# Kernel tuning notes

Measured on AMD Instinct MI355X. Metric: run time of the kernel, lower is better.

The kernel has to match this reference:

```python
import jax, jax.numpy as jnp
import numpy as np

EPS = 1e-5

def _quant_w(w):
    # symmetric per-tensor 8-bit weight quantization with straight-through estimator
    s = jnp.max(jnp.abs(w)) / 127.0
    wq = jnp.round(jnp.clip(w / s, -127.0, 127.0)) * s
    return w + jax.lax.stop_gradient(wq - w)

def _adder_conv(x, w, stride):
    # AdderNet conv: out[b,co,ow] = -sum_{cin,k} |x[b,cin,ow*stride+k] - w[co,cin,k]|
    # x: (B, Cin, L), w: (Co, Cin, K)
    B, Cin, L = x.shape
    Co, _, K = w.shape
    Ow = (L - K) // stride + 1
    idx = jnp.arange(Ow)[:, None] * stride + jnp.arange(K)[None, :]      # (Ow, K)
    patches = x[:, :, idx]                                               # (B, Cin, Ow, K)
    diff = jnp.abs(patches[:, None] - w[None, :, :, None, :])            # (B, Co, Cin, Ow, K)
    return -diff.sum(axis=(2, 4))                                        # (B, Co, Ow)

def _bn(x, p):
    # eval-mode BatchNorm; x: (B,C,W), p: (4,C) = [gamma, beta, running_mean, running_var]
    g, b, m, v = p
    return (x - m[:, None]) * (g[:, None] * jax.lax.rsqrt(v[:, None] + EPS)) + b[:, None]

def _bn_params(key, c):
    k1, k2, k3, k4 = jax.random.split(key, 4)
    g = jax.random.uniform(k1, (c,)) + 0.5
    b = 0.1 * jax.random.normal(k2, (c,))
    m = 0.1 * jax.random.normal(k3, (c,))
    v = jax.random.uniform(k4, (c,)) + 0.5
    return jnp.stack([g, b, m, v]).astype(jnp.float32)

def setup_inputs() -> dict:
    key = jax.random.key(0)
    ks = jax.random.split(key, 22)
    B = 8192
    w = lambda k, shp: (0.1 * jax.random.normal(k, shp)).astype(jnp.float32)
    return {
        'x': jax.random.normal(ks[0], (B, 1, 1, 256), dtype=jnp.float32),
        'w_pre1': w(ks[1], (5, 1, 13)),   'bn_pre1': _bn_params(ks[2], 5),
        'w_pre2': w(ks[3], (10, 5, 9)),   'bn_pre2': _bn_params(ks[4], 10),
        'w_r1':   w(ks[5], (10, 10, 1)),  'bn_r1':   _bn_params(ks[6], 10),
        'w_r2':   w(ks[7], (10, 10, 1)),  'bn_r2':   _bn_params(ks[8], 10),
        'w_o1a':  w(ks[9], (70, 140, 1)), 'bn_o1a':  _bn_params(ks[10], 70),
        'w_o1b':  w(ks[11], (30, 70, 1)), 'bn_o1b':  _bn_params(ks[12], 30),
        'w_o1c':  w(ks[13], (1, 30, 1)),  'bn_o1c':  _bn_params(ks[14], 1),
        'w_o2a':  w(ks[15], (70, 140, 1)),'bn_o2a':  _bn_params(ks[16], 70),
        'w_o2b':  w(ks[17], (30, 70, 1)), 'bn_o2b':  _bn_params(ks[18], 30),
        'w_o2c':  w(ks[19], (1, 30, 1)),  'bn_o2c':  _bn_params(ks[20], 1),
    }

def reference(x, w_pre1, bn_pre1, w_pre2, bn_pre2, w_r1, bn_r1, w_r2, bn_r2,
              w_o1a, bn_o1a, w_o1b, bn_o1b, w_o1c, bn_o1c,
              w_o2a, bn_o2a, w_o2b, bn_o2b, w_o2c, bn_o2c):
    relu = jax.nn.relu
    B = x.shape[0]
    h = x.reshape(B, 1, 256)                                  # height dim is 1 -> 1D
    h = relu(_bn(_adder_conv(h, _quant_w(w_pre1), 5), bn_pre1))   # (B,5,49)
    h = relu(_bn(_adder_conv(h, _quant_w(w_pre2), 3), bn_pre2))   # (B,10,14)
    # ResBlock
    t = relu(_bn(_adder_conv(h, _quant_w(w_r1), 1), bn_r1))
    t = _bn(_adder_conv(t, _quant_w(w_r2), 1), bn_r2)
    h = relu(t + h)                                           # (B,10,14)
    f = h.reshape(B, 140, 1)                                  # flatten to channels
    # O1 branch (amplitude-weighted average lifetime)
    a = relu(_bn(_adder_conv(f, _quant_w(w_o1a), 1), bn_o1a))
    a = relu(_bn(_adder_conv(a, _quant_w(w_o1b), 1), bn_o1b))
    a = relu(_bn(_adder_conv(a, _quant_w(w_o1c), 1), bn_o1c))
    tau_amp = a.reshape(-1)                                   # (B,)
    # O2 branch (intensity-weighted average lifetime)
    b = relu(_bn(_adder_conv(f, _quant_w(w_o2a), 1), bn_o2a))
    b = relu(_bn(_adder_conv(b, _quant_w(w_o2b), 1), bn_o2b))
    b = relu(_bn(_adder_conv(b, _quant_w(w_o2c), 1), bn_o2c))
    tau_inten = b.reshape(-1)                                 # (B,)
    return (tau_amp, tau_inten)
```

## Files before the change

kernel.cpp:

```cpp
#include <hip/hip_runtime.h>

#define TPB 256
#define EPB 8
#define H1S 246
#define ES  280

#define WQ1   0
#define WQ2   65
#define WR1Q  515
#define WR2Q  615
#define WCQ   715
#define WSB   779
#define SMALL_N 1253
#define WQAT  1280
#define WQBT  20880

#define SB_P1 0
#define SB_P2 10
#define SB_R1 30
#define SB_R2 50
#define SB_A1 70
#define SB_B1 210
#define SB_C1 270
#define SB_A2 272
#define SB_B2 412
#define SB_C2 472

#define GFOLD(bn, C, OFF)                                                     \
  if (tid < (C)) {                                                            \
    float gg = (bn)[tid], bb = (bn)[(C) + tid];                               \
    float mm = (bn)[2 * (C) + tid], vv = (bn)[3 * (C) + tid];                 \
    float sc = gg / sqrtf(vv + 1e-5f);                                        \
    sbp[(OFF) + tid] = sc;                                                    \
    sbp[(OFF) + (C) + tid] = bb - mm * sc;                                    \
  }

extern "C" __global__ __launch_bounds__(256)
void prep(const float* __restrict__ w1,  const float* __restrict__ bnp1,
          const float* __restrict__ w2,  const float* __restrict__ bnp2,
          const float* __restrict__ wr1, const float* __restrict__ bnr1,
          const float* __restrict__ wr2, const float* __restrict__ bnr2,
          const float* __restrict__ wa1, const float* __restrict__ bna1,
          const float* __restrict__ wb1, const float* __restrict__ bnb1,
          const float* __restrict__ wc1, const float* __restrict__ bnc1,
          const float* __restrict__ wa2, const float* __restrict__ bna2,
          const float* __restrict__ wb2, const float* __restrict__ bnb2,
          const float* __restrict__ wc2, const float* __restrict__ bnc2,
          float* __restrict__ ws)
{
  __shared__ float s_red[4];
  const int tid = threadIdx.x;
  const int b = blockIdx.x;

  if (b == 10) {
    float* sbp = ws + WSB;
    GFOLD(bnp1, 5, SB_P1)  GFOLD(bnp2, 10, SB_P2)
    GFOLD(bnr1, 10, SB_R1) GFOLD(bnr2, 10, SB_R2)
    GFOLD(bna1, 70, SB_A1) GFOLD(bnb1, 30, SB_B1) GFOLD(bnc1, 1, SB_C1)
    GFOLD(bna2, 70, SB_A2) GFOLD(bnb2, 30, SB_B2) GFOLD(bnc2, 1, SB_C2)
    return;
  }

  const float* src; int n; int mode; int rofs; float* dst = ws;
  int ofs = 0;
  switch (b) {
    case 0: src = w1;  ofs = WQ1;      n = 65;   mode = 0; rofs = 0;  break;
    case 1: src = w2;  ofs = WQ2;      n = 450;  mode = 0; rofs = 0;  break;
    case 2: src = wr1; ofs = WR1Q;     n = 100;  mode = 0; rofs = 0;  break;
    case 3: src = wr2; ofs = WR2Q;     n = 100;  mode = 0; rofs = 0;  break;
    case 4: src = wa1; ofs = WQAT;     n = 9800; mode = 1; rofs = 0;  break;
    case 5: src = wb1; ofs = WQBT;     n = 2100; mode = 2; rofs = 0;  break;
    case 6: src = wc1; ofs = WCQ;      n = 30;   mode = 0; rofs = 0;  break;
    case 7: src = wa2; ofs = WQAT;     n = 9800; mode = 1; rofs = 70; break;
    case 8: src = wb2; ofs = WQBT;     n = 2100; mode = 2; rofs = 30; break;
    default:src = wc2; ofs = WCQ + 32; n = 30;   mode = 0; rofs = 0;  break;
  }

  float m = 0.f;
  for (int i = tid; i < n; i += 256) m = fmaxf(m, fabsf(src[i]));
#pragma unroll
  for (int off = 32; off > 0; off >>= 1)
    m = fmaxf(m, __shfl_down(m, off, 64));
  if ((tid & 63) == 0) s_red[tid >> 6] = m;
  __syncthreads();
  m = fmaxf(fmaxf(s_red[0], s_red[1]), fmaxf(s_red[2], s_red[3]));

  float s = m / 127.0f;
  for (int i = tid; i < n; i += 256) {
    float w = src[i];
    float q = rintf(fminf(fmaxf(w / s, -127.f), 127.f)) * s;
    if (mode == 0) {
      dst[ofs + i] = q;
    } else if (mode == 1) {
      int r = i / 140 + rofs, c = i % 140;
      dst[ofs + ((c >> 2) * 140 + r) * 4 + (c & 3)] = q;
    } else {
      int r = i / 70 + rofs, c = i % 70;
      dst[ofs + ((c >> 1) * 60 + r) * 2 + (c & 1)] = q;
    }
  }
}

extern "C" __global__ __launch_bounds__(TPB, 4)
void taunet(const float* __restrict__ x, const float* __restrict__ ws,
            float* __restrict__ out, int B)
{
  __shared__ __align__(16) float s_h1[EPB * H1S];
  __shared__ __align__(16) float s_e[EPB * ES];
  __shared__ __align__(16) float s_small[SMALL_N];

  const int tid = threadIdx.x;
  const int g  = tid >> 5;
  const int l  = tid & 31;
  const int ln = tid & 63;
  const int wv = tid >> 6;
  const int gp = 2 * wv;
  const int elem = blockIdx.x * EPB + g;

  for (int i = ln; i < SMALL_N; i += 64) s_small[i] = ws[i];

  {
    const float4* xb = (const float4*)x;
#pragma unroll
    for (int it = 0; it < 2; ++it) {
      int e = gp + it;
      int ge = blockIdx.x * EPB + e;
      if (ge < B) {
        float4 v = xb[ge * 64 + ln];
        *(float4*)&s_e[e * ES + ln * 4] = v;
      }
    }
  }

  const float* sb = &s_small[WSB];

  {
    const float* xe = &s_e[g * ES];
#pragma unroll
    for (int rep = 0; rep < 2; ++rep) {
      int p = l + 32 * rep;
      bool act = p < 49;
      int ps = act ? p : 0;
      float win[13];
#pragma unroll
      for (int k = 0; k < 13; ++k) win[k] = xe[5 * ps + k];
#pragma unroll
      for (int ci = 0; ci < 5; ++ci) {
        float a0 = 0.f, a1 = 0.f;
#pragma unroll
        for (int k = 0; k < 13; ++k) {
          float d = fabsf(win[k] - s_small[WQ1 + ci * 13 + k]);
          if (k & 1) a1 += d; else a0 += d;
        }
        float v = fmaxf(fmaf(-(a0 + a1), sb[SB_P1 + ci], sb[SB_P1 + 5 + ci]), 0.f);
        if (act) s_h1[g * H1S + ci * 49 + ps] = v;
      }
    }
  }

  {
    const int ch = l >> 4;
    const int ow16 = l & 15;
    const bool act = ow16 < 14;
    const int ow = act ? ow16 : 0;
    const float* h1b = &s_h1[g * H1S];
    float acc[5] = {0.f, 0.f, 0.f, 0.f, 0.f};
#pragma unroll
    for (int ci = 0; ci < 5; ++ci) {
      float w9[9];
#pragma unroll
      for (int k = 0; k < 9; ++k) w9[k] = h1b[ci * 49 + 3 * ow + k];
#pragma unroll
      for (int c = 0; c < 5; ++c) {
        int co = ch * 5 + c;
        float s0 = 0.f, s1 = 0.f;
#pragma unroll
        for (int k = 0; k < 9; ++k) {
          float d = fabsf(w9[k] - s_small[WQ2 + co * 45 + ci * 9 + k]);
          if (k & 1) s1 += d; else s0 += d;
        }
        acc[c] += s0 + s1;
      }
    }
#pragma unroll
    for (int c = 0; c < 5; ++c) {
      int co = ch * 5 + c;
      float v = fmaxf(fmaf(-acc[c], sb[SB_P2 + co], sb[SB_P2 + 10 + co]), 0.f);
      if (act) s_e[g * ES + co * 14 + ow] = v;
    }
  }

#pragma unroll
  for (int j = 0; j < 5; ++j) {
    int idx = l + 32 * j;
    if (idx < 140) {
      int co = idx / 14, ow = idx % 14;
      float a0 = 0.f, a1 = 0.f;
#pragma unroll
      for (int ci = 0; ci < 10; ++ci) {
        float d = fabsf(s_e[g * ES + ci * 14 + ow] - s_small[WR1Q + co * 10 + ci]);
        if (ci & 1) a1 += d; else a0 += d;
      }
      s_e[g * ES + 140 + idx] =
          fmaxf(fmaf(-(a0 + a1), sb[SB_R1 + co], sb[SB_R1 + 10 + co]), 0.f);
    }
  }

#pragma unroll
  for (int j = 0; j < 5; ++j) {
    int idx = l + 32 * j;
    if (idx < 140) {
      int co = idx / 14, ow = idx % 14;
      float a0 = 0.f, a1 = 0.f;
#pragma unroll
      for (int ci = 0; ci < 10; ++ci) {
        float d = fabsf(s_e[g * ES + 140 + ci * 14 + ow] - s_small[WR2Q + co * 10 + ci]);
        if (ci & 1) a1 += d; else a0 += d;
      }
      float t2 = fmaf(-(a0 + a1), sb[SB_R2 + co], sb[SB_R2 + 10 + co]);
      s_e[g * ES + idx] = fmaxf(t2 + s_e[g * ES + idx], 0.f);
    }
  }

  {
    const float* hb0 = &s_e[gp * ES];
    const float* hb1 = &s_e[(gp + 1) * ES];

    for (int ps = 0; ps < 3; ++ps) {
      int cl = ln + 64 * ps;
      bool act = cl < 140;
      int cls = act ? cl : 0;
      float a0 = 0.f, a1 = 0.f, a2 = 0.f, a3 = 0.f;
      float b0 = 0.f, b1 = 0.f, b2 = 0.f, b3 = 0.f;
#pragma unroll 4
      for (int cb = 0; cb < 35; ++cb) {
        float4 w4 = *(const float4*)&ws[WQAT + (cb * 140 + cls) * 4];
        float4 h4 = *(const float4*)&hb0[cb * 4];
        float4 k4 = *(const float4*)&hb1[cb * 4];
        a0 += fabsf(h4.x - w4.x);
        a1 += fabsf(h4.y - w4.y);
        a2 += fabsf(h4.z - w4.z);
        a3 += fabsf(h4.w - w4.w);
        b0 += fabsf(k4.x - w4.x);
        b1 += fabsf(k4.y - w4.y);
        b2 += fabsf(k4.z - w4.z);
        b3 += fabsf(k4.w - w4.w);
      }
      if (act) {
        int co  = cls < 70 ? cls : cls - 70;
        int off = cls < 70 ? SB_A1 : SB_A2;
        float sc = sb[off + co], bi = sb[off + 70 + co];
        float sadA = (a0 + a1) + (a2 + a3);
        float sadB = (b0 + b1) + (b2 + b3);
        s_h1[gp * H1S + cls]       = fmaxf(fmaf(-sadA, sc, bi), 0.f);
        s_h1[(gp + 1) * H1S + cls] = fmaxf(fmaf(-sadB, sc, bi), 0.f);
      }
    }

    {
      bool act = ln < 60;
      int rl = act ? ln : 0;
      int br = rl >= 30;
      int co = br ? rl - 30 : rl;
      const float* h0 = &s_h1[gp * H1S + br * 70];
      const float* h1 = &s_h1[(gp + 1) * H1S + br * 70];
      int off = br ? SB_B2 : SB_B1;
      float a0 = 0.f, a1 = 0.f, b0 = 0.f, b1 = 0.f;
#pragma unroll 8
      for (int ci = 0; ci < 35; ++ci) {
        float2 w2v = *(const float2*)&ws[WQBT + (ci * 60 + rl) * 2];
        a0 += fabsf(h0[2 * ci]     - w2v.x);
        a1 += fabsf(h0[2 * ci + 1] - w2v.y);
        b0 += fabsf(h1[2 * ci]     - w2v.x);
        b1 += fabsf(h1[2 * ci + 1] - w2v.y);
      }
      if (act) {
        float sc = sb[off + co], bi = sb[off + 30 + co];
        s_e[gp * ES + 140 + rl]       = fmaxf(fmaf(-(a0 + a1), sc, bi), 0.f);
        s_e[(gp + 1) * ES + 140 + rl] = fmaxf(fmaf(-(b0 + b1), sc, bi), 0.f);
      }
    }

    for (int br = 0; br < 2; ++br) {
      float d = 0.f;
      if (l < 30)
        d = fabsf(s_e[g * ES + 140 + br * 30 + l] - s_small[WCQ + br * 32 + l]);
#pragma unroll
      for (int off = 16; off > 0; off >>= 1)
        d += __shfl_down(d, off, 32);
      if (l == 0 && elem < B) {
        int sbC = br ? SB_C2 : SB_C1;
        out[br * B + elem] = fmaxf(fmaf(-d, sb[sbC], sb[sbC + 1]), 0.f);
      }
    }
  }
}

extern "C" void kernel_launch(void* const* d_in, const int* in_sizes, int n_in,
                              void* d_out, int out_size, void* d_ws, size_t ws_size,
                              hipStream_t stream) {
  const float* x    = (const float*)d_in[0];
  const float* w1   = (const float*)d_in[1];
  const float* bnp1 = (const float*)d_in[2];
  const float* w2   = (const float*)d_in[3];
  const float* bnp2 = (const float*)d_in[4];
  const float* wr1  = (const float*)d_in[5];
  const float* bnr1 = (const float*)d_in[6];
  const float* wr2  = (const float*)d_in[7];
  const float* bnr2 = (const float*)d_in[8];
  const float* wa1  = (const float*)d_in[9];
  const float* bna1 = (const float*)d_in[10];
  const float* wb1  = (const float*)d_in[11];
  const float* bnb1 = (const float*)d_in[12];
  const float* wc1  = (const float*)d_in[13];
  const float* bnc1 = (const float*)d_in[14];
  const float* wa2  = (const float*)d_in[15];
  const float* bna2 = (const float*)d_in[16];
  const float* wb2  = (const float*)d_in[17];
  const float* bnb2 = (const float*)d_in[18];
  const float* wc2  = (const float*)d_in[19];
  const float* bnc2 = (const float*)d_in[20];

  float* ws = (float*)d_ws;
  int B = in_sizes[0] / 256;
  int blocks = (B + EPB - 1) / EPB;

  hipLaunchKernelGGL(prep, dim3(11), dim3(256), 0, stream,
                     w1, bnp1, w2, bnp2, wr1, bnr1, wr2, bnr2,
                     wa1, bna1, wb1, bnb1, wc1, bnc1,
                     wa2, bna2, wb2, bnb2, wc2, bnc2, ws);

  hipLaunchKernelGGL(taunet, dim3(blocks), dim3(TPB), 0, stream,
                     x, ws, (float*)d_out, B);
}
```

Baseline: 141.6 us.

## Read uniform weights via scalar loads and keep the residual block in registers

Weights that are uniform across a wave (stage 1 and 2 filters, residual weights, BN scale/bias) are now read directly from global memory, so they can become scalar loads instead of LDS reads. Only the tail of the small table is still staged in LDS. Stage 2 is reorganized so each lane computes all 10 channels for one output position. The two residual 1x1 adder convolutions then run entirely in registers, without LDS round trips. The 140-wide O1/O2 first layer handles three rows per lane in one loop, so each activation float4 is loaded once and reused. In exchange, stage 2 leaves more lanes idle and register pressure rises.

```diff
diff --git a/kernel.cpp b/kernel.cpp
--- a/kernel.cpp
+++ b/kernel.cpp
@@ -117,7 +117,7 @@
   const int gp = 2 * wv;
   const int elem = blockIdx.x * EPB + g;
 
-  for (int i = ln; i < SMALL_N; i += 64) s_small[i] = ws[i];
+  for (int i = WCQ + ln; i < SMALL_N; i += 64) s_small[i] = ws[i];
 
   {
     const float4* xb = (const float4*)x;
@@ -132,8 +132,6 @@
     }
   }
 
-  const float* sb = &s_small[WSB];
-
   {
     const float* xe = &s_e[g * ES];
 #pragma unroll
@@ -149,111 +147,110 @@
         float a0 = 0.f, a1 = 0.f;
 #pragma unroll
         for (int k = 0; k < 13; ++k) {
-          float d = fabsf(win[k] - s_small[WQ1 + ci * 13 + k]);
+          float d = fabsf(win[k] - ws[WQ1 + ci * 13 + k]);
           if (k & 1) a1 += d; else a0 += d;
         }
-        float v = fmaxf(fmaf(-(a0 + a1), sb[SB_P1 + ci], sb[SB_P1 + 5 + ci]), 0.f);
+        float v = fmaxf(fmaf(-(a0 + a1), ws[WSB + SB_P1 + ci],
+                             ws[WSB + SB_P1 + 5 + ci]), 0.f);
         if (act) s_h1[g * H1S + ci * 49 + ps] = v;
       }
     }
   }
 
+  float h2r[10];
   {
-    const int ch = l >> 4;
-    const int ow16 = l & 15;
-    const bool act = ow16 < 14;
-    const int ow = act ? ow16 : 0;
+    const bool act = l < 14;
+    const int ow = act ? l : 0;
     const float* h1b = &s_h1[g * H1S];
-    float acc[5] = {0.f, 0.f, 0.f, 0.f, 0.f};
+    float acc[10] = {0.f,0.f,0.f,0.f,0.f,0.f,0.f,0.f,0.f,0.f};
 #pragma unroll
     for (int ci = 0; ci < 5; ++ci) {
       float w9[9];
 #pragma unroll
       for (int k = 0; k < 9; ++k) w9[k] = h1b[ci * 49 + 3 * ow + k];
 #pragma unroll
-      for (int c = 0; c < 5; ++c) {
-        int co = ch * 5 + c;
+      for (int co = 0; co < 10; ++co) {
         float s0 = 0.f, s1 = 0.f;
 #pragma unroll
         for (int k = 0; k < 9; ++k) {
-          float d = fabsf(w9[k] - s_small[WQ2 + co * 45 + ci * 9 + k]);
+          float d = fabsf(w9[k] - ws[WQ2 + co * 45 + ci * 9 + k]);
           if (k & 1) s1 += d; else s0 += d;
         }
-        acc[c] += s0 + s1;
-      }
-    }
-#pragma unroll
-    for (int c = 0; c < 5; ++c) {
-      int co = ch * 5 + c;
-      float v = fmaxf(fmaf(-acc[c], sb[SB_P2 + co], sb[SB_P2 + 10 + co]), 0.f);
-      if (act) s_e[g * ES + co * 14 + ow] = v;
-    }
-  }
-
-#pragma unroll
-  for (int j = 0; j < 5; ++j) {
-    int idx = l + 32 * j;
-    if (idx < 140) {
-      int co = idx / 14, ow = idx % 14;
-      float a0 = 0.f, a1 = 0.f;
-#pragma unroll
-      for (int ci = 0; ci < 10; ++ci) {
-        float d = fabsf(s_e[g * ES + ci * 14 + ow] - s_small[WR1Q + co * 10 + ci]);
-        if (ci & 1) a1 += d; else a0 += d;
-      }
-      s_e[g * ES + 140 + idx] =
-          fmaxf(fmaf(-(a0 + a1), sb[SB_R1 + co], sb[SB_R1 + 10 + co]), 0.f);
-    }
-  }
-
-#pragma unroll
-  for (int j = 0; j < 5; ++j) {
-    int idx = l + 32 * j;
-    if (idx < 140) {
-      int co = idx / 14, ow = idx % 14;
-      float a0 = 0.f, a1 = 0.f;
-#pragma unroll
-      for (int ci = 0; ci < 10; ++ci) {
-        float d = fabsf(s_e[g * ES + 140 + ci * 14 + ow] - s_small[WR2Q + co * 10 + ci]);
-        if (ci & 1) a1 += d; else a0 += d;
-      }
-      float t2 = fmaf(-(a0 + a1), sb[SB_R2 + co], sb[SB_R2 + 10 + co]);
-      s_e[g * ES + idx] = fmaxf(t2 + s_e[g * ES + idx], 0.f);
-    }
+        acc[co] += s0 + s1;
+      }
+    }
+#pragma unroll
+    for (int co = 0; co < 10; ++co)
+      h2r[co] = fmaxf(fmaf(-acc[co], ws[WSB + SB_P2 + co],
+                           ws[WSB + SB_P2 + 10 + co]), 0.f);
+  }
+
+  float t1r[10];
+#pragma unroll
+  for (int co = 0; co < 10; ++co) {
+    float a0 = 0.f, a1 = 0.f;
+#pragma unroll
+    for (int ci = 0; ci < 10; ++ci) {
+      float d = fabsf(h2r[ci] - ws[WR1Q + co * 10 + ci]);
+      if (ci & 1) a1 += d; else a0 += d;
+    }
+    t1r[co] = fmaxf(fmaf(-(a0 + a1), ws[WSB + SB_R1 + co],
+                         ws[WSB + SB_R1 + 10 + co]), 0.f);
+  }
+
+#pragma unroll
+  for (int co = 0; co < 10; ++co) {
+    float a0 = 0.f, a1 = 0.f;
+#pragma unroll
+    for (int ci = 0; ci < 10; ++ci) {
+      float d = fabsf(t1r[ci] - ws[WR2Q + co * 10 + ci]);
+      if (ci & 1) a1 += d; else a0 += d;
+    }
+    float t2 = fmaf(-(a0 + a1), ws[WSB + SB_R2 + co], ws[WSB + SB_R2 + 10 + co]);
+    float h = fmaxf(t2 + h2r[co], 0.f);
+    if (l < 14) s_e[g * ES + co * 14 + l] = h;
   }
 
   {
     const float* hb0 = &s_e[gp * ES];
     const float* hb1 = &s_e[(gp + 1) * ES];
 
-    for (int ps = 0; ps < 3; ++ps) {
-      int cl = ln + 64 * ps;
-      bool act = cl < 140;
-      int cls = act ? cl : 0;
-      float a0 = 0.f, a1 = 0.f, a2 = 0.f, a3 = 0.f;
-      float b0 = 0.f, b1 = 0.f, b2 = 0.f, b3 = 0.f;
-#pragma unroll 4
-      for (int cb = 0; cb < 35; ++cb) {
-        float4 w4 = *(const float4*)&ws[WQAT + (cb * 140 + cls) * 4];
-        float4 h4 = *(const float4*)&hb0[cb * 4];
-        float4 k4 = *(const float4*)&hb1[cb * 4];
-        a0 += fabsf(h4.x - w4.x);
-        a1 += fabsf(h4.y - w4.y);
-        a2 += fabsf(h4.z - w4.z);
-        a3 += fabsf(h4.w - w4.w);
-        b0 += fabsf(k4.x - w4.x);
-        b1 += fabsf(k4.y - w4.y);
-        b2 += fabsf(k4.z - w4.z);
-        b3 += fabsf(k4.w - w4.w);
-      }
+    const int r2 = (ln + 128 > 139) ? 139 : ln + 128;
+    float accA[3][4], accB[3][4];
+#pragma unroll
+    for (int p = 0; p < 3; ++p)
+#pragma unroll
+      for (int j = 0; j < 4; ++j) { accA[p][j] = 0.f; accB[p][j] = 0.f; }
+    const int rows[3] = {ln, ln + 64, r2};
+#pragma unroll 2
+    for (int cb = 0; cb < 35; ++cb) {
+      float4 h4 = *(const float4*)&hb0[cb * 4];
+      float4 k4 = *(const float4*)&hb1[cb * 4];
+#pragma unroll
+      for (int p = 0; p < 3; ++p) {
+        float4 w4 = *(const float4*)&ws[WQAT + (cb * 140 + rows[p]) * 4];
+        accA[p][0] += fabsf(h4.x - w4.x);
+        accA[p][1] += fabsf(h4.y - w4.y);
+        accA[p][2] += fabsf(h4.z - w4.z);
+        accA[p][3] += fabsf(h4.w - w4.w);
+        accB[p][0] += fabsf(k4.x - w4.x);
+        accB[p][1] += fabsf(k4.y - w4.y);
+        accB[p][2] += fabsf(k4.z - w4.z);
+        accB[p][3] += fabsf(k4.w - w4.w);
+      }
+    }
+#pragma unroll
+    for (int p = 0; p < 3; ++p) {
+      int cl = rows[p];
+      bool act = (p < 2) || (ln < 12);
       if (act) {
-        int co  = cls < 70 ? cls : cls - 70;
-        int off = cls < 70 ? SB_A1 : SB_A2;
-        float sc = sb[off + co], bi = sb[off + 70 + co];
-        float sadA = (a0 + a1) + (a2 + a3);
-        float sadB = (b0 + b1) + (b2 + b3);
-        s_h1[gp * H1S + cls]       = fmaxf(fmaf(-sadA, sc, bi), 0.f);
-        s_h1[(gp + 1) * H1S + cls] = fmaxf(fmaf(-sadB, sc, bi), 0.f);
+        int co  = cl < 70 ? cl : cl - 70;
+        int off = cl < 70 ? SB_A1 : SB_A2;
+        float sc = s_small[WSB + off + co], bi = s_small[WSB + off + 70 + co];
+        float sadA = (accA[p][0] + accA[p][1]) + (accA[p][2] + accA[p][3]);
+        float sadB = (accB[p][0] + accB[p][1]) + (accB[p][2] + accB[p][3]);
+        s_h1[gp * H1S + cl]       = fmaxf(fmaf(-sadA, sc, bi), 0.f);
+        s_h1[(gp + 1) * H1S + cl] = fmaxf(fmaf(-sadB, sc, bi), 0.f);
       }
     }
 
@@ -275,7 +272,7 @@
         b1 += fabsf(h1[2 * ci + 1] - w2v.y);
       }
       if (act) {
-        float sc = sb[off + co], bi = sb[off + 30 + co];
+        float sc = s_small[WSB + off + co], bi = s_small[WSB + off + 30 + co];
         s_e[gp * ES + 140 + rl]       = fmaxf(fmaf(-(a0 + a1), sc, bi), 0.f);
         s_e[(gp + 1) * ES + 140 + rl] = fmaxf(fmaf(-(b0 + b1), sc, bi), 0.f);
       }
@@ -290,7 +287,8 @@
         d += __shfl_down(d, off, 32);
       if (l == 0 && elem < B) {
         int sbC = br ? SB_C2 : SB_C1;
-        out[br * B + elem] = fmaxf(fmaf(-d, sb[sbC], sb[sbC + 1]), 0.f);
+        out[br * B + elem] =
+            fmaxf(fmaf(-d, ws[WSB + sbC], ws[WSB + sbC + 1]), 0.f);
       }
     }
   }
```

After: 146.3 us. +3.3%, slower.
